# Kernel optimization log

Hardware: AMD Instinct MI355X
Metric: run time of the kernel (lower is better)

The kernel has to match this reference:

```python
import jax, jax.numpy as jnp
import numpy as np

B, S, E, H, FF = 2, 2048, 768, 12, 3072
D = E // H
EPS = 1e-5


def setup_inputs() -> dict:
    key = jax.random.key(0)
    ks = jax.random.split(key, 12)
    sc = lambda n: 1.0 / np.sqrt(n)
    return {
        "x": jax.random.normal(ks[0], (B, S, E), jnp.float32),
        "wq": jax.random.normal(ks[1], (E, E), jnp.float32) * sc(E),
        "wk": jax.random.normal(ks[2], (E, E), jnp.float32) * sc(E),
        "wv": jax.random.normal(ks[3], (E, E), jnp.float32) * sc(E),
        "wo": jax.random.normal(ks[4], (E, E), jnp.float32) * sc(E),
        "bo": jax.random.normal(ks[5], (E,), jnp.float32) * 0.02,
        "w1": jax.random.normal(ks[6], (FF, E), jnp.float32) * sc(E),
        "b1": jax.random.normal(ks[7], (FF,), jnp.float32) * 0.02,
        "w2": jax.random.normal(ks[8], (E, FF), jnp.float32) * sc(FF),
        "b2": jax.random.normal(ks[9], (E,), jnp.float32) * 0.02,
        "gamma": jnp.ones((E,), jnp.float32),
        "beta": jnp.zeros((E,), jnp.float32),
    }


def _layernorm(x, g, b):
    mu = jnp.mean(x, axis=-1, keepdims=True)
    var = jnp.mean(jnp.square(x - mu), axis=-1, keepdims=True)
    return (x - mu) * jax.lax.rsqrt(var + EPS) * g + b


def reference(x, wq, wk, wv, wo, bo, w1, b1, w2, b2, gamma, beta):
    res = x
    xn = _layernorm(x, gamma, beta)
    # Q/K/V projections (torch Linear: y = x @ W.T), split into heads
    q = (xn @ wq.T).reshape(B, S, H, D)
    k = (xn @ wk.T).reshape(B, S, H, D)
    v = (xn @ wv.T).reshape(B, S, H, D)
    scale = jnp.sqrt(jnp.float32(D))
    scores = jnp.einsum("bqhd,bkhd->bhqk", q, k) / scale  # [B,H,S,S]
    causal = jnp.tril(jnp.ones((S, S), bool))
    scores = jnp.where(causal, scores, -jnp.inf)
    w = jax.nn.softmax(scores, axis=-1)
    attn = jnp.einsum("bhqk,bkhd->bqhd", w, v).reshape(B, S, E)
    attn = attn @ wo.T + bo
    res = res + attn
    y = _layernorm(res, gamma, beta)  # NOTE: same LayerNorm params reused (as in source)
    h = jax.nn.gelu(y @ w1.T + b1, approximate=False)  # nn.GELU default is exact erf
    ffn = h @ w2.T + b2
    return res + ffn
```

## Files before the change

kernel.cpp:

```cpp
#include <hip/hip_runtime.h>
#include <hip/hip_bf16.h>
#include <math.h>

typedef __bf16 bf16_8 __attribute__((ext_vector_type(8)));
typedef __bf16 bf16_4 __attribute__((ext_vector_type(4)));
typedef float f32x4 __attribute__((ext_vector_type(4)));

#define AS1 __attribute__((address_space(1)))
#define AS3 __attribute__((address_space(3)))

__global__ __launch_bounds__(256) void ln_kernel(
    const float* __restrict__ x, const float* __restrict__ g,
    const float* __restrict__ b, __hip_bfloat16* __restrict__ out, int cols) {
  const int row = blockIdx.x;
  const int t = threadIdx.x;
  float loc[3];
  float s = 0.f, s2 = 0.f;
#pragma unroll
  for (int i = 0; i < 3; ++i) {
    float v = x[(size_t)row * cols + t + i * 256];
    loc[i] = v;
    s += v;
    s2 += v * v;
  }
#pragma unroll
  for (int off = 32; off; off >>= 1) {
    s += __shfl_down(s, off);
    s2 += __shfl_down(s2, off);
  }
  __shared__ float red[2][4];
  const int lane = t & 63, w = t >> 6;
  if (lane == 0) {
    red[0][w] = s;
    red[1][w] = s2;
  }
  __syncthreads();
  s = red[0][0] + red[0][1] + red[0][2] + red[0][3];
  s2 = red[1][0] + red[1][1] + red[1][2] + red[1][3];
  const float mu = s / cols;
  const float var = s2 / cols - mu * mu;
  const float rs = rsqrtf(var + 1e-5f);
  __hip_bfloat16* orow = out + (size_t)row * cols;
#pragma unroll
  for (int i = 0; i < 3; ++i) {
    int c = t + i * 256;
    orow[c] = __hip_bfloat16((loc[i] - mu) * rs * g[c] + b[c]);
  }
}

__global__ __launch_bounds__(256) void reduce_ln(
    const float* __restrict__ x, const float* __restrict__ part, int nz,
    const float* __restrict__ bias, const float* __restrict__ g,
    const float* __restrict__ b, float* __restrict__ res,
    __hip_bfloat16* __restrict__ yout) {
  const int row = blockIdx.x;
  const int t = threadIdx.x;
  const size_t zstride = (size_t)4096 * 768;
  float loc[3];
  float s = 0.f, s2 = 0.f;
#pragma unroll
  for (int i = 0; i < 3; ++i) {
    const int c = t + i * 256;
    const size_t off = (size_t)row * 768 + c;
    float v = x[off] + bias[c];
    for (int z = 0; z < nz; ++z) v += part[(size_t)z * zstride + off];
    res[off] = v;
    loc[i] = v;
    s += v;
    s2 += v * v;
  }
#pragma unroll
  for (int off = 32; off; off >>= 1) {
    s += __shfl_down(s, off);
    s2 += __shfl_down(s2, off);
  }
  __shared__ float red[2][4];
  const int lane = t & 63, w = t >> 6;
  if (lane == 0) {
    red[0][w] = s;
    red[1][w] = s2;
  }
  __syncthreads();
  s = red[0][0] + red[0][1] + red[0][2] + red[0][3];
  s2 = red[1][0] + red[1][1] + red[1][2] + red[1][3];
  const float mu = s / 768.f;
  const float var = s2 / 768.f - mu * mu;
  const float rs = rsqrtf(var + 1e-5f);
#pragma unroll
  for (int i = 0; i < 3; ++i) {
    const int c = t + i * 256;
    yout[(size_t)row * 768 + c] = __hip_bfloat16((loc[i] - mu) * rs * g[c] + b[c]);
  }
}

__global__ __launch_bounds__(256) void reduce_out(
    const float* __restrict__ part, int nz, const float* __restrict__ bias,
    float* __restrict__ res) {
  const int row = blockIdx.x;
  const int t = threadIdx.x;
  const size_t zstride = (size_t)4096 * 768;
#pragma unroll
  for (int i = 0; i < 3; ++i) {
    const int c = t + i * 256;
    const size_t off = (size_t)row * 768 + c;
    float v = res[off] + bias[c];
    for (int z = 0; z < nz; ++z) v += part[(size_t)z * zstride + off];
    res[off] = v;
  }
}

__global__ __launch_bounds__(256) void cvt_multi(
    const float* __restrict__ sa, const float* __restrict__ sb,
    const float* __restrict__ sc, const float* __restrict__ sd,
    __hip_bfloat16* __restrict__ da, __hip_bfloat16* __restrict__ db,
    __hip_bfloat16* __restrict__ dc, __hip_bfloat16* __restrict__ dd) {
  const float* src;
  __hip_bfloat16* dst;
  if (blockIdx.y == 0) { src = sa; dst = da; }
  else if (blockIdx.y == 1) { src = sb; dst = db; }
  else if (blockIdx.y == 2) { src = sc; dst = dc; }
  else { src = sd; dst = dd; }
  const size_t i = ((size_t)blockIdx.x * 256 + threadIdx.x) * 4;
  float4 f = *(const float4*)(src + i);
  bf16_4 o;
  o[0] = (__bf16)f.x; o[1] = (__bf16)f.y; o[2] = (__bf16)f.z; o[3] = (__bf16)f.w;
  *(bf16_4*)((__bf16*)dst + i) = o;
}

template <int MODE, bool BF32>
__global__ __launch_bounds__(256) void gemm_bt(
    const __hip_bfloat16* __restrict__ A, const void* __restrict__ Bx,
    const float* __restrict__ bias, void* __restrict__ out,
    int M, int N, int K, int lda, int ldb, int ldout) {
  constexpr int BM = 128, BN = 128, BK = 64;
  constexpr int LDBP = BF32 ? 72 : BK;
  __shared__ __align__(16) __bf16 As[2][BM * BK];
  __shared__ __align__(16) __bf16 Bs[2][BN * LDBP];
  const int tid = threadIdx.x;
  const int m0 = blockIdx.y * BM;
  const int n0 = blockIdx.x * BN;
  const int wave = tid >> 6;
  const int lane = tid & 63;
  const int quad = lane >> 4;
  const int l16 = lane & 15;
  const int wm = (wave & 1) * 64;
  const int wn = (wave >> 1) * 64;

  int kbase = 0, kcnt = K;
  if constexpr (MODE == 2 || MODE == 3) {
    kcnt = K / gridDim.z;
    kbase = blockIdx.z * kcnt;
  }
  const int nt = kcnt / BK;

  const int srow = lane >> 3;
  const int scol = ((lane & 7) ^ (srow & 7)) * 8;
  const __hip_bfloat16* Ap = A + (size_t)(m0 + wave * 8 + srow) * lda + kbase + scol;
  const __hip_bfloat16* Bpb = nullptr;
  const float* Bpf = nullptr;
  if constexpr (BF32)
    Bpf = (const float*)Bx;
  else
    Bpb = (const __hip_bfloat16*)Bx + (size_t)(n0 + wave * 8 + srow) * ldb + kbase + scol;

  f32x4 acc[4][4] = {};

  auto STAGE = [&](int t, int buf) {
    const int k0 = t * BK;
#pragma unroll
    for (int u = 0; u < 4; ++u) {
      __builtin_amdgcn_global_load_lds(
          (const AS1 void*)(Ap + (size_t)(u * 32) * lda + k0),
          (AS3 void*)(&As[buf][(u * 32 + wave * 8) * BK]), 16, 0, 0);
      if constexpr (!BF32)
        __builtin_amdgcn_global_load_lds(
            (const AS1 void*)(Bpb + (size_t)(u * 32) * ldb + k0),
            (AS3 void*)(&Bs[buf][(u * 32 + wave * 8) * BK]), 16, 0, 0);
    }
    if constexpr (BF32) {
#pragma unroll
      for (int u = 0; u < 4; ++u) {
        int c = u * 256 + tid;
        int row = c >> 3, kc = c & 7;
        const float* src = Bpf + (size_t)(n0 + row) * ldb + kbase + k0 + kc * 8;
        float4 f0 = *(const float4*)src;
        float4 f1 = *(const float4*)(src + 4);
        bf16_8 bv;
        bv[0] = (__bf16)f0.x; bv[1] = (__bf16)f0.y; bv[2] = (__bf16)f0.z; bv[3] = (__bf16)f0.w;
        bv[4] = (__bf16)f1.x; bv[5] = (__bf16)f1.y; bv[6] = (__bf16)f1.z; bv[7] = (__bf16)f1.w;
        *(bf16_8*)(&Bs[buf][row * LDBP + kc * 8]) = bv;
      }
    }
  };

  STAGE(0, 0);
  __syncthreads();
  int cur = 0;
  for (int t = 0; t < nt; ++t) {
    if (t + 1 < nt) STAGE(t + 1, cur ^ 1);
#pragma unroll
    for (int kk = 0; kk < 2; ++kk) {
      bf16_8 af[4], bfr[4];
#pragma unroll
      for (int i = 0; i < 4; ++i)
        af[i] = *(const bf16_8*)(
            &As[cur][(wm + i * 16 + l16) * BK + (((kk * 4 + quad) ^ (l16 & 7)) * 8)]);
#pragma unroll
      for (int j = 0; j < 4; ++j) {
        if constexpr (BF32)
          bfr[j] = *(const bf16_8*)(&Bs[cur][(wn + j * 16 + l16) * LDBP + kk * 32 + quad * 8]);
        else
          bfr[j] = *(const bf16_8*)(
              &Bs[cur][(wn + j * 16 + l16) * BK + (((kk * 4 + quad) ^ (l16 & 7)) * 8)]);
      }
#pragma unroll
      for (int i = 0; i < 4; ++i)
#pragma unroll
        for (int j = 0; j < 4; ++j)
          acc[i][j] =
              __builtin_amdgcn_mfma_f32_16x16x32_bf16(af[i], bfr[j], acc[i][j], 0, 0, 0);
    }
    __syncthreads();
    cur ^= 1;
  }

#pragma unroll
  for (int i = 0; i < 4; ++i) {
#pragma unroll
    for (int j = 0; j < 4; ++j) {
#pragma unroll
      for (int r = 0; r < 4; ++r) {
        const int row = m0 + wm + i * 16 + quad * 4 + r;
        const int col = n0 + wn + j * 16 + l16;
        const float v = acc[i][j][r];
        if constexpr (MODE == 0) {
          const int tsel = n0 / 768;
          const size_t idx = ((size_t)tsel * M + row) * 768 + (col - tsel * 768);
          ((__hip_bfloat16*)out)[idx] = __hip_bfloat16(v);
        } else if constexpr (MODE == 1) {
          float tt = v + bias[col];
          float gl = 0.5f * tt * (1.0f + erff(tt * 0.70710678118654752f));
          ((__hip_bfloat16*)out)[(size_t)row * ldout + col] = __hip_bfloat16(gl);
        } else if constexpr (MODE == 2) {
          float add = v + ((blockIdx.z == 0 && bias) ? bias[col] : 0.f);
          atomicAdd((float*)out + (size_t)row * 768 + col, add);
        } else {
          ((float*)out)[(size_t)blockIdx.z * M * 768 + (size_t)row * 768 + col] = v;
        }
      }
    }
  }
}

__global__ void zero_ctr(int* __restrict__ c) {
  if (threadIdx.x == 0) *c = 0;
}

#define ALDP 72
__global__ __launch_bounds__(256) void attn_mfma(
    const __hip_bfloat16* __restrict__ qb, const __hip_bfloat16* __restrict__ kb,
    const __hip_bfloat16* __restrict__ vb, __hip_bfloat16* __restrict__ ob,
    int* __restrict__ ctr) {
  const int S = 2048, H = 12, E = 768;
  const int tid = threadIdx.x;
  const int wave = tid >> 6;
  const int lane = tid & 63;
  const int quad = lane >> 4;
  const int l16 = lane & 15;

  __shared__ __align__(16) __bf16 Ks[64 * ALDP];
  __shared__ __align__(16) __bf16 Vt[64 * ALDP];
  __shared__ __align__(16) __bf16 Pl[4][16 * ALDP];
  __shared__ int task;

  for (;;) {
    if (tid == 0) task = atomicAdd(ctr, 1);
    __syncthreads();
    const int t = task;
    if (t >= 24 * 32) return;
    const int qblk = 31 - (t / 24);
    const int bh = t - (t / 24) * 24;
    const int b = bh / H, h = bh - b * H;
    const int q0 = qblk * 64;
    const int qw = q0 + wave * 16;
    const size_t base = (size_t)b * S * E + (size_t)h * 64;

    bf16_8 qf[2];
#pragma unroll
    for (int s = 0; s < 2; ++s)
      qf[s] = *(const bf16_8*)(qb + base + (size_t)(qw + l16) * E + s * 32 + quad * 8);

    f32x4 o[4] = {};
    float mq = -1e30f, lq = 0.f;

    for (int kt = 0; kt <= qblk; ++kt) {
      const int k0 = kt * 64;
      __syncthreads();
#pragma unroll
      for (int u = 0; u < 2; ++u) {
        int i = tid + u * 256;
        int kr = i >> 3, kc = i & 7;
        *(bf16_8*)(&Ks[kr * ALDP + kc * 8]) =
            *(const bf16_8*)(kb + base + (size_t)(k0 + kr) * E + kc * 8);
      }
#pragma unroll
      for (int u = 0; u < 2; ++u) {
        int i = tid + u * 256;
        int kr = i & 63, dq = i >> 6;
        bf16_8 vv = *(const bf16_8*)(vb + base + (size_t)(k0 + kr) * E + dq * 8);
#pragma unroll
        for (int j = 0; j < 8; ++j) Vt[(dq * 8 + j) * ALDP + kr] = vv[j];
      }
      __syncthreads();

      f32x4 sc[4] = {};
#pragma unroll
      for (int jj = 0; jj < 4; ++jj)
#pragma unroll
        for (int s = 0; s < 2; ++s) {
          bf16_8 kf = *(const bf16_8*)(&Ks[(jj * 16 + l16) * ALDP + s * 32 + quad * 8]);
          sc[jj] = __builtin_amdgcn_mfma_f32_16x16x32_bf16(kf, qf[s], sc[jj], 0, 0, 0);
        }

      float mx = -1e30f;
#pragma unroll
      for (int jj = 0; jj < 4; ++jj)
#pragma unroll
        for (int r = 0; r < 4; ++r) {
          float v = sc[jj][r] * 0.125f;
          if (kt == qblk && (k0 + jj * 16 + quad * 4 + r) > (qw + l16)) v = -1e30f;
          sc[jj][r] = v;
          mx = fmaxf(mx, v);
        }
      mx = fmaxf(mx, __shfl_xor(mx, 16));
      mx = fmaxf(mx, __shfl_xor(mx, 32));
      const float mn = fmaxf(mq, mx);
      const float corr = __expf(mq - mn);
      mq = mn;
      float sum = 0.f;
#pragma unroll
      for (int jj = 0; jj < 4; ++jj)
#pragma unroll
        for (int r = 0; r < 4; ++r) {
          float p = __expf(sc[jj][r] - mn);
          sc[jj][r] = p;
          sum += p;
        }
      sum += __shfl_xor(sum, 16);
      sum += __shfl_xor(sum, 32);
      lq = lq * corr + sum;
#pragma unroll
      for (int nt2 = 0; nt2 < 4; ++nt2)
#pragma unroll
        for (int r = 0; r < 4; ++r) o[nt2][r] *= corr;

      __bf16* pw = &Pl[wave][0];
#pragma unroll
      for (int jj = 0; jj < 4; ++jj)
#pragma unroll
        for (int r = 0; r < 4; ++r)
          pw[l16 * ALDP + jj * 16 + quad * 4 + r] = (__bf16)sc[jj][r];

#pragma unroll
      for (int s = 0; s < 2; ++s) {
        bf16_8 pf = *(const bf16_8*)(&pw[l16 * ALDP + s * 32 + quad * 8]);
#pragma unroll
        for (int dt = 0; dt < 4; ++dt) {
          bf16_8 vf = *(const bf16_8*)(&Vt[(dt * 16 + l16) * ALDP + s * 32 + quad * 8]);
          o[dt] = __builtin_amdgcn_mfma_f32_16x16x32_bf16(vf, pf, o[dt], 0, 0, 0);
        }
      }
    }

    const float inv = 1.f / lq;
    __bf16* pw = &Pl[wave][0];
#pragma unroll
    for (int dt = 0; dt < 4; ++dt)
#pragma unroll
      for (int r = 0; r < 4; ++r)
        pw[l16 * ALDP + dt * 16 + quad * 4 + r] = (__bf16)(o[dt][r] * inv);
#pragma unroll
    for (int u = 0; u < 2; ++u) {
      int j = lane + u * 64;
      int ql = j >> 3, ch = j & 7;
      bf16_8 ov = *(const bf16_8*)(&pw[ql * ALDP + ch * 8]);
      *(bf16_8*)(ob + base + (size_t)(qw + ql) * E + ch * 8) = ov;
    }
  }
}

extern "C" void kernel_launch(void* const* d_in, const int* in_sizes, int n_in,
                              void* d_out, int out_size, void* d_ws, size_t ws_size,
                              hipStream_t stream) {
  const int Bv = 2, S = 2048, E = 768, FF = 3072;
  const int M = Bv * S;
  const size_t ME = (size_t)M * E;
  const size_t EE = (size_t)E * E;
  const size_t EF = (size_t)E * FF;

  const float* x = (const float*)d_in[0];
  const float* wq = (const float*)d_in[1];
  const float* wk = (const float*)d_in[2];
  const float* wv = (const float*)d_in[3];
  const float* wo = (const float*)d_in[4];
  const float* bo = (const float*)d_in[5];
  const float* w1 = (const float*)d_in[6];
  const float* b1 = (const float*)d_in[7];
  const float* w2 = (const float*)d_in[8];
  const float* b2 = (const float*)d_in[9];
  const float* gamma = (const float*)d_in[10];
  const float* beta = (const float*)d_in[11];

  int* ctr = (int*)d_ws;
  __hip_bfloat16* slot = (__hip_bfloat16*)((char*)d_ws + 256);
  __hip_bfloat16* s0 = slot;
  __hip_bfloat16* s1 = slot + ME;
  __hip_bfloat16* s4 = slot + 4 * ME;
  __hip_bfloat16* s5 = slot + 5 * ME;
  float* pp = (float*)(slot + 5 * ME + 2 * EF);
  float* res = (float*)d_out;

  const size_t need_mid = 256 + (5 * ME + 2 * EF) * sizeof(__hip_bfloat16);
  const size_t need_full = need_mid + 4 * ME * sizeof(float);
  const bool full = ws_size >= need_full;
  const bool mid = ws_size >= need_mid;

  cvt_multi<<<dim3(EE / 1024, 4), 256, 0, stream>>>(
      wq, wk, wv, wo, s4, s4 + EE, s4 + 2 * EE, s4 + 3 * EE);
  if (mid)
    cvt_multi<<<dim3(EF / 1024, 2), 256, 0, stream>>>(
        w1, w2, nullptr, nullptr, s5, s5 + EF, nullptr, nullptr);
  ln_kernel<<<M, 256, 0, stream>>>(x, gamma, beta, s0, E);
  gemm_bt<0, false><<<dim3(18, 32), 256, 0, stream>>>(s0, s4, nullptr, s1, M, 2304, E, E, E, 0);
  zero_ctr<<<1, 64, 0, stream>>>(ctr);
  attn_mfma<<<768, 256, 0, stream>>>(s1, s1 + ME, s1 + 2 * ME, s0, ctr);

  if (full) {
    gemm_bt<3, false><<<dim3(6, 32, 4), 256, 0, stream>>>(
        s0, s4 + 3 * EE, nullptr, pp, M, E, E, E, E, 0);
    reduce_ln<<<M, 256, 0, stream>>>(x, pp, 4, bo, gamma, beta, res, s0);
    gemm_bt<1, false><<<dim3(24, 32), 256, 0, stream>>>(s0, s5, b1, s1, M, FF, E, E, E, FF);
    gemm_bt<3, false><<<dim3(6, 32, 4), 256, 0, stream>>>(
        s1, s5 + EF, nullptr, pp, M, E, FF, FF, FF, 0);
    reduce_out<<<M, 256, 0, stream>>>(pp, 4, b2, res);
  } else {
    hipMemcpyAsync(d_out, x, ME * sizeof(float), hipMemcpyDeviceToDevice, stream);
    gemm_bt<2, false><<<dim3(6, 32, 2), 256, 0, stream>>>(
        s0, s4 + 3 * EE, bo, res, M, E, E, E, E, 0);
    ln_kernel<<<M, 256, 0, stream>>>(res, gamma, beta, s0, E);
    if (mid) {
      gemm_bt<1, false><<<dim3(24, 32), 256, 0, stream>>>(s0, s5, b1, s1, M, FF, E, E, E, FF);
      gemm_bt<2, false><<<dim3(6, 32, 4), 256, 0, stream>>>(
          s1, s5 + EF, b2, res, M, E, FF, FF, FF, 0);
    } else {
      gemm_bt<1, true><<<dim3(24, 32), 256, 0, stream>>>(s0, w1, b1, s1, M, FF, E, E, E, FF);
      cvt_multi<<<dim3(EF / 1024, 1), 256, 0, stream>>>(
          w2, nullptr, nullptr, nullptr, s0, nullptr, nullptr, nullptr);
      gemm_bt<2, false><<<dim3(6, 32, 4), 256, 0, stream>>>(
          s1, s0, b2, res, M, E, FF, FF, FF, 0);
    }
  }
}
```

Baseline: 333.6 us.

## Double-buffer attention K/V tiles with async LDS loads and pre-transposed V

The attention kernel now double-buffers its K and V tiles in shared memory, prefetching the next tile with global_load_lds while the current one is computed, and uses XOR-swizzled layouts to avoid bank conflicts. When enough workspace is available, a separate kernel first transposes V into a per-head [D,S] layout so the attention kernel can load V directly instead of scattering it element by element. It also adds s_setprio around the MFMA blocks and vectorizes the P/output stores to LDS. The cost is an extra transpose kernel launch with its own memory traffic, plus twice the K/V shared-memory footprint, which may reduce occupancy.

```diff
diff --git a/kernel.cpp b/kernel.cpp
--- a/kernel.cpp
+++ b/kernel.cpp
@@ -125,6 +125,33 @@
   bf16_4 o;
   o[0] = (__bf16)f.x; o[1] = (__bf16)f.y; o[2] = (__bf16)f.z; o[3] = (__bf16)f.w;
   *(bf16_4*)((__bf16*)dst + i) = o;
+}
+
+__global__ __launch_bounds__(256) void transpose_v(
+    const __hip_bfloat16* __restrict__ v, __hip_bfloat16* __restrict__ vt) {
+  const int S = 2048, E = 768, H = 12;
+  const int s0 = blockIdx.x * 64;
+  const int bh = blockIdx.y;
+  const int b = bh / H, h = bh - b * H;
+  __shared__ __align__(16) __bf16 T[64 * 72];
+  const int tid = threadIdx.x;
+#pragma unroll
+  for (int u = 0; u < 2; ++u) {
+    int i = tid + u * 256;
+    int sr = i >> 3, c = i & 7;
+    *(bf16_8*)(&T[sr * 72 + c * 8]) =
+        *(const bf16_8*)(v + ((size_t)b * S + s0 + sr) * E + h * 64 + c * 8);
+  }
+  __syncthreads();
+#pragma unroll
+  for (int u = 0; u < 2; ++u) {
+    int i = tid + u * 256;
+    int dr = i >> 3, kc = i & 7;
+    bf16_8 o;
+#pragma unroll
+    for (int e = 0; e < 8; ++e) o[e] = T[(kc * 8 + e) * 72 + dr];
+    *(bf16_8*)(vt + ((size_t)bh * 64 + dr) * S + s0 + kc * 8) = o;
+  }
 }
 
 template <int MODE, bool BF32>
@@ -257,6 +284,7 @@
 }
 
 #define ALDP 72
+template <bool PRE_T>
 __global__ __launch_bounds__(256) void attn_mfma(
     const __hip_bfloat16* __restrict__ qb, const __hip_bfloat16* __restrict__ kb,
     const __hip_bfloat16* __restrict__ vb, __hip_bfloat16* __restrict__ ob,
@@ -268,10 +296,13 @@
   const int quad = lane >> 4;
   const int l16 = lane & 15;
 
-  __shared__ __align__(16) __bf16 Ks[64 * ALDP];
-  __shared__ __align__(16) __bf16 Vt[64 * ALDP];
+  __shared__ __align__(16) __bf16 Ks[2][64 * 64];
+  __shared__ __align__(16) __bf16 Vt[2][64 * 64];
   __shared__ __align__(16) __bf16 Pl[4][16 * ALDP];
   __shared__ int task;
+
+  const int srow8 = lane >> 3;
+  const int csrc = ((lane & 7) ^ srow8) * 8;
 
   for (;;) {
     if (tid == 0) task = atomicAdd(ctr, 1);
@@ -285,6 +316,34 @@
     const int qw = q0 + wave * 16;
     const size_t base = (size_t)b * S * E + (size_t)h * 64;
 
+    auto STAGE = [&](int kts, int buf) {
+      const int k0s = kts * 64;
+#pragma unroll
+      for (int u = 0; u < 2; ++u) {
+        const int trow = wave * 16 + u * 8;
+        __builtin_amdgcn_global_load_lds(
+            (const AS1 void*)(kb + base + (size_t)(k0s + trow + srow8) * E + csrc),
+            (AS3 void*)(&Ks[buf][trow * 64]), 16, 0, 0);
+        if constexpr (PRE_T)
+          __builtin_amdgcn_global_load_lds(
+              (const AS1 void*)(vb + ((size_t)(bh * 64 + trow + srow8)) * S + k0s + csrc),
+              (AS3 void*)(&Vt[buf][trow * 64]), 16, 0, 0);
+      }
+      if constexpr (!PRE_T) {
+#pragma unroll
+        for (int u = 0; u < 2; ++u) {
+          int i = tid + u * 256;
+          int kr = i & 63, dq = i >> 6;
+          bf16_8 vv = *(const bf16_8*)(vb + base + (size_t)(k0s + kr) * E + dq * 8);
+#pragma unroll
+          for (int j = 0; j < 8; ++j) {
+            int drow = dq * 8 + j;
+            Vt[buf][drow * 64 + (((kr >> 3) ^ (drow & 7)) * 8) + (kr & 7)] = vv[j];
+          }
+        }
+      }
+    };
+
     bf16_8 qf[2];
 #pragma unroll
     for (int s = 0; s < 2; ++s)
@@ -293,34 +352,25 @@
     f32x4 o[4] = {};
     float mq = -1e30f, lq = 0.f;
 
+    STAGE(0, 0);
+    __syncthreads();
+    int cur = 0;
+
     for (int kt = 0; kt <= qblk; ++kt) {
       const int k0 = kt * 64;
-      __syncthreads();
-#pragma unroll
-      for (int u = 0; u < 2; ++u) {
-        int i = tid + u * 256;
-        int kr = i >> 3, kc = i & 7;
-        *(bf16_8*)(&Ks[kr * ALDP + kc * 8]) =
-            *(const bf16_8*)(kb + base + (size_t)(k0 + kr) * E + kc * 8);
-      }
-#pragma unroll
-      for (int u = 0; u < 2; ++u) {
-        int i = tid + u * 256;
-        int kr = i & 63, dq = i >> 6;
-        bf16_8 vv = *(const bf16_8*)(vb + base + (size_t)(k0 + kr) * E + dq * 8);
-#pragma unroll
-        for (int j = 0; j < 8; ++j) Vt[(dq * 8 + j) * ALDP + kr] = vv[j];
-      }
-      __syncthreads();
+      if (kt < qblk) STAGE(kt + 1, cur ^ 1);
 
       f32x4 sc[4] = {};
+      __builtin_amdgcn_s_setprio(1);
 #pragma unroll
       for (int jj = 0; jj < 4; ++jj)
 #pragma unroll
         for (int s = 0; s < 2; ++s) {
-          bf16_8 kf = *(const bf16_8*)(&Ks[(jj * 16 + l16) * ALDP + s * 32 + quad * 8]);
+          bf16_8 kf = *(const bf16_8*)(
+              &Ks[cur][(jj * 16 + l16) * 64 + (((s * 4 + quad) ^ (l16 & 7)) * 8)]);
           sc[jj] = __builtin_amdgcn_mfma_f32_16x16x32_bf16(kf, qf[s], sc[jj], 0, 0, 0);
         }
+      __builtin_amdgcn_s_setprio(0);
 
       float mx = -1e30f;
 #pragma unroll
@@ -356,29 +406,39 @@
 
       __bf16* pw = &Pl[wave][0];
 #pragma unroll
-      for (int jj = 0; jj < 4; ++jj)
-#pragma unroll
-        for (int r = 0; r < 4; ++r)
-          pw[l16 * ALDP + jj * 16 + quad * 4 + r] = (__bf16)sc[jj][r];
+      for (int jj = 0; jj < 4; ++jj) {
+        bf16_4 p4;
+#pragma unroll
+        for (int r = 0; r < 4; ++r) p4[r] = (__bf16)sc[jj][r];
+        *(bf16_4*)(&pw[l16 * ALDP + jj * 16 + quad * 4]) = p4;
+      }
 
 #pragma unroll
       for (int s = 0; s < 2; ++s) {
         bf16_8 pf = *(const bf16_8*)(&pw[l16 * ALDP + s * 32 + quad * 8]);
+        __builtin_amdgcn_s_setprio(1);
 #pragma unroll
         for (int dt = 0; dt < 4; ++dt) {
-          bf16_8 vf = *(const bf16_8*)(&Vt[(dt * 16 + l16) * ALDP + s * 32 + quad * 8]);
+          bf16_8 vf = *(const bf16_8*)(
+              &Vt[cur][(dt * 16 + l16) * 64 + (((s * 4 + quad) ^ (l16 & 7)) * 8)]);
           o[dt] = __builtin_amdgcn_mfma_f32_16x16x32_bf16(vf, pf, o[dt], 0, 0, 0);
         }
-      }
+        __builtin_amdgcn_s_setprio(0);
+      }
+
+      __syncthreads();
+      cur ^= 1;
     }
 
     const float inv = 1.f / lq;
     __bf16* pw = &Pl[wave][0];
 #pragma unroll
-    for (int dt = 0; dt < 4; ++dt)
-#pragma unroll
-      for (int r = 0; r < 4; ++r)
-        pw[l16 * ALDP + dt * 16 + quad * 4 + r] = (__bf16)(o[dt][r] * inv);
+    for (int dt = 0; dt < 4; ++dt) {
+      bf16_4 o4;
+#pragma unroll
+      for (int r = 0; r < 4; ++r) o4[r] = (__bf16)(o[dt][r] * inv);
+      *(bf16_4*)(&pw[l16 * ALDP + dt * 16 + quad * 4]) = o4;
+    }
 #pragma unroll
     for (int u = 0; u < 2; ++u) {
       int j = lane + u * 64;
@@ -418,6 +478,7 @@
   __hip_bfloat16* s4 = slot + 4 * ME;
   __hip_bfloat16* s5 = slot + 5 * ME;
   float* pp = (float*)(slot + 5 * ME + 2 * EF);
+  __hip_bfloat16* vt = (__hip_bfloat16*)pp;
   float* res = (float*)d_out;
 
   const size_t need_mid = 256 + (5 * ME + 2 * EF) * sizeof(__hip_bfloat16);
@@ -433,7 +494,12 @@
   ln_kernel<<<M, 256, 0, stream>>>(x, gamma, beta, s0, E);
   gemm_bt<0, false><<<dim3(18, 32), 256, 0, stream>>>(s0, s4, nullptr, s1, M, 2304, E, E, E, 0);
   zero_ctr<<<1, 64, 0, stream>>>(ctr);
-  attn_mfma<<<768, 256, 0, stream>>>(s1, s1 + ME, s1 + 2 * ME, s0, ctr);
+  if (full) {
+    transpose_v<<<dim3(32, 24), 256, 0, stream>>>(s1 + 2 * ME, vt);
+    attn_mfma<true><<<768, 256, 0, stream>>>(s1, s1 + ME, vt, s0, ctr);
+  } else {
+    attn_mfma<false><<<768, 256, 0, stream>>>(s1, s1 + ME, s1 + 2 * ME, s0, ctr);
+  }
 
   if (full) {
     gemm_bt<3, false><<<dim3(6, 32, 4), 256, 0, stream>>>(
```

Result: no change. 332.8 us (-0.2%).
